# Performance work log

Measured on AMD Instinct MI355X. Metric: run time of the kernel, lower is better.

The kernel has to match this reference:

```python
import jax, jax.numpy as jnp
import numpy as np

B, S, HID = 1, 2048, 2048
NH, NKV, HD = 32, 8, 64  # query heads, kv heads, head dim
NEG = -1e9


def rotate_half(x):
    d = x.shape[-1] // 2
    return jnp.concatenate([-x[..., d:], x[..., :d]], axis=-1)


def setup_inputs() -> dict:
    key = jax.random.key(0)
    ks = jax.random.split(key, 8)
    hidden_states = jax.random.normal(ks[0], (B, S, HID), dtype=jnp.float32)
    # RoPE angles: realistic cos/sin tables (B, S, HD)
    inv_freq = 1.0 / (10000.0 ** (np.arange(0, HD, 2, dtype=np.float32) / HD))
    pos = np.arange(S, dtype=np.float32)
    ang = pos[:, None] * inv_freq[None, :]            # (S, HD/2)
    ang = np.concatenate([ang, ang], axis=-1)          # (S, HD)
    cos = jnp.broadcast_to(jnp.cos(ang)[None], (B, S, HD)).astype(jnp.float32)
    sin = jnp.broadcast_to(jnp.sin(ang)[None], (B, S, HD)).astype(jnp.float32)
    # additive causal mask (B, 1, S, S)
    causal = jnp.where(jnp.tril(jnp.ones((S, S), dtype=bool)), 0.0, NEG).astype(jnp.float32)
    attention_mask = jnp.broadcast_to(causal[None, None], (B, 1, S, S))
    std = 0.02
    Wq = jax.random.normal(ks[1], (NH * HD, HID), dtype=jnp.float32) * std
    Wk = jax.random.normal(ks[2], (NKV * HD, HID), dtype=jnp.float32) * std
    Wv = jax.random.normal(ks[3], (NKV * HD, HID), dtype=jnp.float32) * std
    Wo = jax.random.normal(ks[4], (HID, NH * HD), dtype=jnp.float32) * std
    return {"hidden_states": hidden_states, "cos": cos, "sin": sin,
            "attention_mask": attention_mask, "Wq": Wq, "Wk": Wk, "Wv": Wv, "Wo": Wo}


def reference(hidden_states, cos, sin, attention_mask, Wq, Wk, Wv, Wo):
    scaling = HD ** -0.5
    n_rep = NH // NKV
    # projections -> (B, H, S, D)
    q = jnp.einsum('bsh,qh->bsq', hidden_states, Wq).reshape(B, S, NH, HD).transpose(0, 2, 1, 3)
    k = jnp.einsum('bsh,qh->bsq', hidden_states, Wk).reshape(B, S, NKV, HD).transpose(0, 2, 1, 3)
    v = jnp.einsum('bsh,qh->bsq', hidden_states, Wv).reshape(B, S, NKV, HD).transpose(0, 2, 1, 3)
    # RoPE (cos/sin broadcast over head dim via [:, None])
    c, s = cos[:, None], sin[:, None]
    q = q * c + rotate_half(q) * s
    k = k * c + rotate_half(k) * s
    # GQA repeat_kv
    k = jnp.repeat(k, n_rep, axis=1)
    v = jnp.repeat(v, n_rep, axis=1)
    # eager attention
    attn_weights = jnp.einsum('bhqd,bhkd->bhqk', q, k) * scaling
    attn_weights = attn_weights + attention_mask
    attn_weights = jax.nn.softmax(attn_weights.astype(jnp.float32), axis=-1).astype(q.dtype)
    attn_output = jnp.einsum('bhqk,bhkd->bhqd', attn_weights, v)
    attn_output = attn_output.transpose(0, 2, 1, 3).reshape(B, S, NH * HD)
    attn_output = jnp.einsum('bsq,hq->bsh', attn_output, Wo)
    return attn_output, attn_weights
```

## Files before the change

kernel.cpp:

```cpp
#include <hip/hip_runtime.h>

#define S_LEN 2048
#define NH 32
#define NKV 8
#define HD 64
#define QH_DIM (NH * HD)
#define QKV_DIM 3072
#define K_OFF 2048
#define V_OFF 2560
#define LOG2E 1.44269504089f

typedef __attribute__((ext_vector_type(8))) __bf16 bf16x8;
typedef __attribute__((ext_vector_type(4))) float fx4;
typedef __attribute__((ext_vector_type(8))) unsigned short ush8;

__device__ __forceinline__ unsigned short f2bf(float f) {
  return __builtin_bit_cast(unsigned short, (__bf16)f);
}
__device__ __forceinline__ float bf2f(unsigned short h) {
  unsigned int u = ((unsigned int)h) << 16;
  return __builtin_bit_cast(float, u);
}
__device__ __forceinline__ fx4 zero4() {
  fx4 z; z[0] = 0.f; z[1] = 0.f; z[2] = 0.f; z[3] = 0.f; return z;
}

#define MFMA16(a, b, c) __builtin_amdgcn_mfma_f32_16x16x32_bf16((a), (b), (c), 0, 0, 0)

__device__ __forceinline__ void gl16(const void* g, void* l) {
  __builtin_amdgcn_global_load_lds((const __attribute__((address_space(1))) void*)g,
                                   (__attribute__((address_space(3))) void*)l, 16, 0, 0);
}

__global__ __launch_bounds__(256) void cast5(const float* __restrict__ s0, unsigned short* d0, int n0,
                                             const float* __restrict__ s1, unsigned short* d1, int n1,
                                             const float* __restrict__ s2, unsigned short* d2, int n2,
                                             const float* __restrict__ s3, unsigned short* d3, int n3,
                                             const float* __restrict__ s4, unsigned short* d4, int n4) {
  int i = blockIdx.x * 256 + threadIdx.x;
  const float* s;
  unsigned short* d;
  if (i < n0) { s = s0; d = d0; }
  else if ((i -= n0) < n1) { s = s1; d = d1; }
  else if ((i -= n1) < n2) { s = s2; d = d2; }
  else if ((i -= n2) < n3) { s = s3; d = d3; }
  else if ((i -= n3) < n4) { s = s4; d = d4; }
  else return;
  float4 v = ((const float4*)s)[i];
  ushort4 o;
  o.x = f2bf(v.x); o.y = f2bf(v.y); o.z = f2bf(v.z); o.w = f2bf(v.w);
  ((ushort4*)d)[i] = o;
}

__global__ __launch_bounds__(512) void gemm_split(const unsigned short* __restrict__ A,
                                                  const unsigned short* __restrict__ B,
                                                  unsigned short* __restrict__ Part,
                                                  int M, int N, int K) {
  __shared__ unsigned short As[2][128 * 32];
  __shared__ unsigned short Bs[2][128 * 32];
  const int tid = threadIdx.x;
  const int bn = blockIdx.x * 128, bm = blockIdx.y * 128;
  const int kslice = blockIdx.z;
  const int KH = K >> 1;
  const size_t koff = (size_t)kslice * KH;
  const int lane = tid & 63, wid = tid >> 6;
  const int lo = lane & 15, g = lane >> 4;
  const int wr = wid >> 2, wc = wid & 3;

  fx4 acc[4][2];
#pragma unroll
  for (int i = 0; i < 4; i++)
#pragma unroll
    for (int j = 0; j < 2; j++) acc[i][j] = zero4();

  const int srow = tid >> 2;
  const int cg = (tid & 3) ^ ((srow >> 1) & 3);
  const unsigned short* apg = &A[(size_t)(bm + srow) * K + koff + cg * 8];
  const unsigned short* bpg = &B[(size_t)(bn + srow) * K + koff + cg * 8];

  const int arow = wr * 64 + lo;
  const int brow = wc * 32 + lo;
  const int sc = (g ^ ((lo >> 1) & 3)) * 8;

#define G_STAGE(s, k0)                  \
  do {                                  \
    gl16(apg + (k0), &As[s][tid * 8]);  \
    gl16(bpg + (k0), &Bs[s][tid * 8]);  \
  } while (0)

#define G_COMPUTE(s)                                                   \
  do {                                                                 \
    bf16x8 af[4], bb[2];                                               \
    _Pragma("unroll") for (int mi = 0; mi < 4; mi++)                   \
        af[mi] = *(const bf16x8*)&As[s][(arow + mi * 16) * 32 + sc];   \
    _Pragma("unroll") for (int nj = 0; nj < 2; nj++)                   \
        bb[nj] = *(const bf16x8*)&Bs[s][(brow + nj * 16) * 32 + sc];   \
    _Pragma("unroll") for (int mi = 0; mi < 4; mi++)                   \
        _Pragma("unroll") for (int nj = 0; nj < 2; nj++)               \
            acc[mi][nj] = MFMA16(af[mi], bb[nj], acc[mi][nj]);         \
  } while (0)

  const int NT = KH >> 5;
  G_STAGE(0, 0);
  __syncthreads();
  int cur = 0;
  for (int t = 0; t < NT - 1; ++t) {
    G_STAGE(cur ^ 1, (t + 1) * 32);
    G_COMPUTE(cur);
    __syncthreads();
    cur ^= 1;
  }
  G_COMPUTE(cur);
#undef G_STAGE
#undef G_COMPUTE

  unsigned short* const pb = &Part[(size_t)kslice * M * N];
#pragma unroll
  for (int mi = 0; mi < 4; mi++)
#pragma unroll
    for (int nj = 0; nj < 2; nj++)
#pragma unroll
      for (int r = 0; r < 4; r++) {
        int row = bm + wr * 64 + mi * 16 + g * 4 + r;
        int col = bn + wc * 32 + nj * 16 + lo;
        pb[(size_t)row * N + col] = f2bf(acc[mi][nj][r]);
      }
}

__global__ __launch_bounds__(256) void combine_qkv(const unsigned short* __restrict__ P0,
                                                   const unsigned short* __restrict__ P1,
                                                   unsigned short* __restrict__ qkv,
                                                   const float* __restrict__ cosp,
                                                   const float* __restrict__ sinp,
                                                   unsigned short* __restrict__ Vt) {
  __shared__ unsigned short t[64][72];
  const int b = blockIdx.x;
  if (b < 2560) {
    int idx = b * 256 + threadIdx.x;
    int j = idx & 7;
    int tt = idx >> 3;
    int head = tt % 40;
    int s = tt / 40;
    const float scale = (head < 32) ? 0.125f * LOG2E : 1.0f;
    const size_t base = (size_t)s * QKV_DIM + head * 64 + j * 4;
    ushort4 a0l = *(const ushort4*)&P0[base];
    ushort4 a1l = *(const ushort4*)&P1[base];
    ushort4 a0h = *(const ushort4*)&P0[base + 32];
    ushort4 a1h = *(const ushort4*)&P1[base + 32];
    float xl0 = bf2f(a0l.x) + bf2f(a1l.x), xl1 = bf2f(a0l.y) + bf2f(a1l.y);
    float xl2 = bf2f(a0l.z) + bf2f(a1l.z), xl3 = bf2f(a0l.w) + bf2f(a1l.w);
    float xh0 = bf2f(a0h.x) + bf2f(a1h.x), xh1 = bf2f(a0h.y) + bf2f(a1h.y);
    float xh2 = bf2f(a0h.z) + bf2f(a1h.z), xh3 = bf2f(a0h.w) + bf2f(a1h.w);
    fx4 cl = *(const fx4*)&cosp[s * 64 + j * 4];
    fx4 ch = *(const fx4*)&cosp[s * 64 + 32 + j * 4];
    fx4 sl = *(const fx4*)&sinp[s * 64 + j * 4];
    fx4 sh = *(const fx4*)&sinp[s * 64 + 32 + j * 4];
    ushort4 ol, oh;
    ol.x = f2bf((xl0 * cl[0] - xh0 * sl[0]) * scale);
    ol.y = f2bf((xl1 * cl[1] - xh1 * sl[1]) * scale);
    ol.z = f2bf((xl2 * cl[2] - xh2 * sl[2]) * scale);
    ol.w = f2bf((xl3 * cl[3] - xh3 * sl[3]) * scale);
    oh.x = f2bf((xh0 * ch[0] + xl0 * sh[0]) * scale);
    oh.y = f2bf((xh1 * ch[1] + xl1 * sh[1]) * scale);
    oh.z = f2bf((xh2 * ch[2] + xl2 * sh[2]) * scale);
    oh.w = f2bf((xh3 * ch[3] + xl3 * sh[3]) * scale);
    *(ushort4*)&qkv[base] = ol;
    *(ushort4*)&qkv[base + 32] = oh;
  } else {
    const int tid = threadIdx.x;
    const int bb = b - 2560;
    const int cb = (bb & 7) * 64;
    const int rb = (bb >> 3) * 64;
#pragma unroll
    for (int rr = 0; rr < 2; rr++) {
      int row = rr * 32 + (tid >> 3);
      int c8 = (tid & 7) * 8;
      const size_t src = (size_t)(rb + row) * QKV_DIM + V_OFF + cb + c8;
      ush8 a = *(const ush8*)&P0[src];
      ush8 c = *(const ush8*)&P1[src];
      ush8 o;
#pragma unroll
      for (int j = 0; j < 8; j++) o[j] = f2bf(bf2f(a[j]) + bf2f(c[j]));
      *(ush8*)&t[row][c8] = o;
    }
    __syncthreads();
#pragma unroll
    for (int rr = 0; rr < 2; rr++) {
      int col = rr * 32 + (tid >> 3);
      int r8 = (tid & 7) * 8;
      ush8 o;
#pragma unroll
      for (int j = 0; j < 8; j++) o[j] = t[r8 + j][col];
      *(ush8*)&Vt[(size_t)(cb + col) * S_LEN + rb + r8] = o;
    }
  }
}

__global__ __launch_bounds__(256) void combine_wo(const unsigned short* __restrict__ P0,
                                                  const unsigned short* __restrict__ P1,
                                                  float* __restrict__ out) {
  const int i = blockIdx.x * 256 + threadIdx.x;
  const size_t base = (size_t)i * 8;
  ush8 a = *(const ush8*)&P0[base];
  ush8 b = *(const ush8*)&P1[base];
  fx4 o0, o1;
#pragma unroll
  for (int j = 0; j < 4; j++) o0[j] = bf2f(a[j]) + bf2f(b[j]);
#pragma unroll
  for (int j = 0; j < 4; j++) o1[j] = bf2f(a[4 + j]) + bf2f(b[4 + j]);
  *(fx4*)&out[base] = o0;
  *(fx4*)&out[base + 4] = o1;
}

__global__ __launch_bounds__(256) void attn_kernel(const unsigned short* __restrict__ Q,
                                                   const unsigned short* __restrict__ Kb,
                                                   const unsigned short* __restrict__ Vt,
                                                   float* __restrict__ P,
                                                   unsigned short* __restrict__ AO) {
  __shared__ unsigned short pls[16][2048];
  __shared__ float lred[4][16];
  const int h = blockIdx.x;
  const int rt = 127 - blockIdx.y;
  const int hkv = h >> 2;
  const int wid = threadIdx.x >> 6, lane = threadIdx.x & 63;
  const int lo = lane & 15, g = lane >> 4;
  const int rowb = rt * 16;
  const int nkt = (rt + 4) >> 2;
  const int qg = rowb + lo;
  char* const plsb = (char*)pls;
  const int swz = (lo & 7) << 4;

  {
    const int zc0 = nkt * 64;
    const int nz4 = (S_LEN - zc0) >> 2;
    for (int idx = threadIdx.x; idx < 16 * nz4; idx += 256) {
      const int r = idx / nz4;
      const int c = idx - r * nz4;
      __builtin_nontemporal_store(zero4(),
          (fx4*)&P[((size_t)h * S_LEN + rowb + r) * S_LEN + zc0 + c * 4]);
    }
  }

  const bf16x8 qa0 = *(const bf16x8*)&Q[(size_t)qg * QKV_DIM + h * HD + g * 8];
  const bf16x8 qa1 = *(const bf16x8*)&Q[(size_t)qg * QKV_DIM + h * HD + 32 + g * 8];

  float l = 0.f;
  {
    bf16x8 kc0[4], kc1[4];
    if (wid < nkt) {
#pragma unroll
      for (int nj = 0; nj < 4; nj++) {
        const int kcol = wid * 64 + nj * 16 + lo;
        kc0[nj] = *(const bf16x8*)&Kb[(size_t)kcol * QKV_DIM + hkv * HD + g * 8];
        kc1[nj] = *(const bf16x8*)&Kb[(size_t)kcol * QKV_DIM + hkv * HD + 32 + g * 8];
      }
    }
    for (int kt = wid; kt < nkt; kt += 4) {
      bf16x8 kn0[4], kn1[4];
      if (kt + 4 < nkt) {
#pragma unroll
        for (int nj = 0; nj < 4; nj++) {
          const int kcol = (kt + 4) * 64 + nj * 16 + lo;
          kn0[nj] = *(const bf16x8*)&Kb[(size_t)kcol * QKV_DIM + hkv * HD + g * 8];
          kn1[nj] = *(const bf16x8*)&Kb[(size_t)kcol * QKV_DIM + hkv * HD + 32 + g * 8];
        }
      }
      fx4 acc[4];
      __builtin_amdgcn_s_setprio(1);
#pragma unroll
      for (int nj = 0; nj < 4; nj++) {
        acc[nj] = MFMA16(kc0[nj], qa0, zero4());
        acc[nj] = MFMA16(kc1[nj], qa1, acc[nj]);
      }
      __builtin_amdgcn_s_setprio(0);
      const bool diag = (kt == nkt - 1);
#pragma unroll
      for (int nj = 0; nj < 4; nj++) {
        float e[4];
#pragma unroll
        for (int r = 0; r < 4; r++) {
          float v = exp2f(acc[nj][r]);
          if (diag && (kt * 64 + nj * 16 + g * 4 + r > qg)) v = 0.f;
          l += v;
          e[r] = v;
        }
        unsigned int w0 = (unsigned int)f2bf(e[0]) | ((unsigned int)f2bf(e[1]) << 16);
        unsigned int w1 = (unsigned int)f2bf(e[2]) | ((unsigned int)f2bf(e[3]) << 16);
        uint2 w; w.x = w0; w.y = w1;
        *(uint2*)(plsb + lo * 4096 + ((kt * 128 + nj * 32 + g * 8) ^ swz)) = w;
      }
#pragma unroll
      for (int j = 0; j < 4; j++) { kc0[j] = kn0[j]; kc1[j] = kn1[j]; }
    }
  }
  l += __shfl_xor(l, 16);
  l += __shfl_xor(l, 32);
  if (lane < 16) lred[wid][lo] = l;

  const unsigned short* const vrow = &Vt[(size_t)(hkv * HD + wid * 16 + lo) * S_LEN];
  bf16x8 vc0 = *(const bf16x8*)&vrow[g * 8];
  bf16x8 vc1 = *(const bf16x8*)&vrow[32 + g * 8];

  __syncthreads();

  float pinv[4];
#pragma unroll
  for (int it = 0; it < 4; it++) {
    const int rho = it * 4 + g;
    pinv[it] = 1.f / (lred[0][rho] + lred[1][rho] + lred[2][rho] + lred[3][rho]);
  }
  float* const pbase = &P[((size_t)h * S_LEN + rowb) * S_LEN];

  fx4 oacc = zero4();
  for (int kt = 0; kt < nkt; ++kt) {
    bf16x8 vn0, vn1;
    if (kt + 1 < nkt) {
      vn0 = *(const bf16x8*)&vrow[(kt + 1) * 64 + g * 8];
      vn1 = *(const bf16x8*)&vrow[(kt + 1) * 64 + 32 + g * 8];
    }
    bf16x8 pa0 = *(const bf16x8*)(plsb + lo * 4096 + ((kt * 128 + g * 16) ^ swz));
    bf16x8 pa1 = *(const bf16x8*)(plsb + lo * 4096 + ((kt * 128 + 64 + g * 16) ^ swz));
    __builtin_amdgcn_s_setprio(1);
    oacc = MFMA16(pa0, vc0, oacc);
    oacc = MFMA16(pa1, vc1, oacc);
    __builtin_amdgcn_s_setprio(0);
    if ((kt & 3) == wid) {
#pragma unroll
      for (int it = 0; it < 4; it++) {
        const int rho = it * 4 + g;
        ushort4 b4 = *(const ushort4*)(plsb + rho * 4096 +
                                       ((kt * 128 + lo * 8) ^ ((rho & 7) << 4)));
        fx4 pv;
        pv[0] = bf2f(b4.x) * pinv[it]; pv[1] = bf2f(b4.y) * pinv[it];
        pv[2] = bf2f(b4.z) * pinv[it]; pv[3] = bf2f(b4.w) * pinv[it];
        __builtin_nontemporal_store(pv,
            (fx4*)&pbase[(size_t)rho * S_LEN + kt * 64 + lo * 4]);
      }
    }
    vc0 = vn0; vc1 = vn1;
  }

#pragma unroll
  for (int r = 0; r < 4; r++) {
    const int q = g * 4 + r;
    const float linv = 1.f / (lred[0][q] + lred[1][q] + lred[2][q] + lred[3][q]);
    AO[(size_t)(rowb + q) * QH_DIM + h * HD + wid * 16 + lo] = f2bf(oacc[r] * linv);
  }
}

extern "C" void kernel_launch(void* const* d_in, const int* in_sizes, int n_in,
                              void* d_out, int out_size, void* d_ws, size_t ws_size,
                              hipStream_t stream) {
  const float* hs = (const float*)d_in[0];
  const float* cosp = (const float*)d_in[1];
  const float* sinp = (const float*)d_in[2];
  const float* Wq = (const float*)d_in[4];
  const float* Wk = (const float*)d_in[5];
  const float* Wv = (const float*)d_in[6];
  const float* Wo = (const float*)d_in[7];

  char* w = (char*)d_ws;
  unsigned short* wo_bf   = (unsigned short*)(w);
  unsigned short* ao_bf   = (unsigned short*)(w + (((size_t)9) << 20));
  unsigned short* hs_bf   = (unsigned short*)(w + (((size_t)18) << 20));
  unsigned short* wqkv_bf = (unsigned short*)(w + (((size_t)27) << 20));
  unsigned short* qkv_bf  = (unsigned short*)(w + (((size_t)40) << 20));
  unsigned short* vt_bf   = (unsigned short*)(w + (((size_t)53) << 20));
  unsigned short* wop     = hs_bf;

  float* out0 = (float*)d_out;
  float* P = out0 + (size_t)S_LEN * QH_DIM;
  const size_t P_BYTES = (size_t)NH * S_LEN * S_LEN * 4;
  const size_t QKVP_BYTES = (size_t)2 * S_LEN * QKV_DIM * 2;
  unsigned short* qkvp = (unsigned short*)((char*)P + P_BYTES - QKVP_BYTES);

  cast5<<<14336, 256, 0, stream>>>(hs, hs_bf, 1048576,
                                   Wq, wqkv_bf, 1048576,
                                   Wk, wqkv_bf + (size_t)K_OFF * 2048, 262144,
                                   Wv, wqkv_bf + (size_t)V_OFF * 2048, 262144,
                                   Wo, wo_bf, 1048576);

  gemm_split<<<dim3(QKV_DIM / 128, 16, 2), 512, 0, stream>>>(hs_bf, wqkv_bf, qkvp,
                                                             2048, QKV_DIM, 2048);

  combine_qkv<<<2816, 256, 0, stream>>>(qkvp, qkvp + (size_t)S_LEN * QKV_DIM,
                                        qkv_bf, cosp, sinp, vt_bf);

  attn_kernel<<<dim3(NH, 128), 256, 0, stream>>>(qkv_bf, qkv_bf + K_OFF, vt_bf, P, ao_bf);

  gemm_split<<<dim3(16, 16, 2), 512, 0, stream>>>(ao_bf, wo_bf, wop, 2048, 2048, 2048);

  combine_wo<<<2048, 256, 0, stream>>>(wop, wop + (size_t)S_LEN * QH_DIM, out0);
}
```

Before: 260.4 us.

## Use eight waves per attention block with split-K PV and LDS reduction

Attention blocks grow from 4 to 8 waves. The QK tiles are strided across 8 waves, and the PV accumulation is split into two parity halves over key tiles. The halves are combined through a shared-memory buffer before writing the attention output. The goal is more latency hiding per block on the exp/store-heavy path; the cost is an extra sync, extra LDS, and fewer registers per thread. The GEMM launch bounds also gain a min-blocks hint, which may constrain registers.

```diff
diff --git a/kernel.cpp b/kernel.cpp
--- a/kernel.cpp
+++ b/kernel.cpp
@@ -52,10 +52,10 @@
   ((ushort4*)d)[i] = o;
 }
 
-__global__ __launch_bounds__(512) void gemm_split(const unsigned short* __restrict__ A,
-                                                  const unsigned short* __restrict__ B,
-                                                  unsigned short* __restrict__ Part,
-                                                  int M, int N, int K) {
+__global__ __launch_bounds__(512, 6) void gemm_split(const unsigned short* __restrict__ A,
+                                                     const unsigned short* __restrict__ B,
+                                                     unsigned short* __restrict__ Part,
+                                                     int M, int N, int K) {
   __shared__ unsigned short As[2][128 * 32];
   __shared__ unsigned short Bs[2][128 * 32];
   const int tid = threadIdx.x;
@@ -212,13 +212,14 @@
   *(fx4*)&out[base + 4] = o1;
 }
 
-__global__ __launch_bounds__(256) void attn_kernel(const unsigned short* __restrict__ Q,
-                                                   const unsigned short* __restrict__ Kb,
-                                                   const unsigned short* __restrict__ Vt,
-                                                   float* __restrict__ P,
-                                                   unsigned short* __restrict__ AO) {
+__global__ __launch_bounds__(512, 4) void attn_kernel(const unsigned short* __restrict__ Q,
+                                                      const unsigned short* __restrict__ Kb,
+                                                      const unsigned short* __restrict__ Vt,
+                                                      float* __restrict__ P,
+                                                      unsigned short* __restrict__ AO) {
   __shared__ unsigned short pls[16][2048];
-  __shared__ float lred[4][16];
+  __shared__ float lred[8][16];
+  __shared__ fx4 obuf[4][64];
   const int h = blockIdx.x;
   const int rt = 127 - blockIdx.y;
   const int hkv = h >> 2;
@@ -233,7 +234,7 @@
   {
     const int zc0 = nkt * 64;
     const int nz4 = (S_LEN - zc0) >> 2;
-    for (int idx = threadIdx.x; idx < 16 * nz4; idx += 256) {
+    for (int idx = threadIdx.x; idx < 16 * nz4; idx += 512) {
       const int r = idx / nz4;
       const int c = idx - r * nz4;
       __builtin_nontemporal_store(zero4(),
@@ -255,12 +256,12 @@
         kc1[nj] = *(const bf16x8*)&Kb[(size_t)kcol * QKV_DIM + hkv * HD + 32 + g * 8];
       }
     }
-    for (int kt = wid; kt < nkt; kt += 4) {
+    for (int kt = wid; kt < nkt; kt += 8) {
       bf16x8 kn0[4], kn1[4];
-      if (kt + 4 < nkt) {
+      if (kt + 8 < nkt) {
 #pragma unroll
         for (int nj = 0; nj < 4; nj++) {
-          const int kcol = (kt + 4) * 64 + nj * 16 + lo;
+          const int kcol = (kt + 8) * 64 + nj * 16 + lo;
           kn0[nj] = *(const bf16x8*)&Kb[(size_t)kcol * QKV_DIM + hkv * HD + g * 8];
           kn1[nj] = *(const bf16x8*)&Kb[(size_t)kcol * QKV_DIM + hkv * HD + 32 + g * 8];
         }
@@ -297,9 +298,11 @@
   l += __shfl_xor(l, 32);
   if (lane < 16) lred[wid][lo] = l;
 
-  const unsigned short* const vrow = &Vt[(size_t)(hkv * HD + wid * 16 + lo) * S_LEN];
-  bf16x8 vc0 = *(const bf16x8*)&vrow[g * 8];
-  bf16x8 vc1 = *(const bf16x8*)&vrow[32 + g * 8];
+  const int d0 = (wid & 3) * 16;
+  const int par = wid >> 2;
+  const unsigned short* const vrow = &Vt[(size_t)(hkv * HD + d0 + lo) * S_LEN];
+  bf16x8 vc0 = *(const bf16x8*)&vrow[par * 64 + g * 8];
+  bf16x8 vc1 = *(const bf16x8*)&vrow[par * 64 + 32 + g * 8];
 
   __syncthreads();
 
@@ -307,16 +310,17 @@
 #pragma unroll
   for (int it = 0; it < 4; it++) {
     const int rho = it * 4 + g;
-    pinv[it] = 1.f / (lred[0][rho] + lred[1][rho] + lred[2][rho] + lred[3][rho]);
+    pinv[it] = 1.f / (lred[0][rho] + lred[1][rho] + lred[2][rho] + lred[3][rho] +
+                      lred[4][rho] + lred[5][rho] + lred[6][rho] + lred[7][rho]);
   }
   float* const pbase = &P[((size_t)h * S_LEN + rowb) * S_LEN];
 
   fx4 oacc = zero4();
-  for (int kt = 0; kt < nkt; ++kt) {
+  for (int kt = par; kt < nkt; kt += 2) {
     bf16x8 vn0, vn1;
-    if (kt + 1 < nkt) {
-      vn0 = *(const bf16x8*)&vrow[(kt + 1) * 64 + g * 8];
-      vn1 = *(const bf16x8*)&vrow[(kt + 1) * 64 + 32 + g * 8];
+    if (kt + 2 < nkt) {
+      vn0 = *(const bf16x8*)&vrow[(kt + 2) * 64 + g * 8];
+      vn1 = *(const bf16x8*)&vrow[(kt + 2) * 64 + 32 + g * 8];
     }
     bf16x8 pa0 = *(const bf16x8*)(plsb + lo * 4096 + ((kt * 128 + g * 16) ^ swz));
     bf16x8 pa1 = *(const bf16x8*)(plsb + lo * 4096 + ((kt * 128 + 64 + g * 16) ^ swz));
@@ -324,7 +328,7 @@
     oacc = MFMA16(pa0, vc0, oacc);
     oacc = MFMA16(pa1, vc1, oacc);
     __builtin_amdgcn_s_setprio(0);
-    if ((kt & 3) == wid) {
+    if (((kt >> 1) & 3) == (wid & 3)) {
 #pragma unroll
       for (int it = 0; it < 4; it++) {
         const int rho = it * 4 + g;
@@ -340,11 +344,17 @@
     vc0 = vn0; vc1 = vn1;
   }
 
-#pragma unroll
-  for (int r = 0; r < 4; r++) {
-    const int q = g * 4 + r;
-    const float linv = 1.f / (lred[0][q] + lred[1][q] + lred[2][q] + lred[3][q]);
-    AO[(size_t)(rowb + q) * QH_DIM + h * HD + wid * 16 + lo] = f2bf(oacc[r] * linv);
+  if (par == 1) obuf[wid & 3][lane] = oacc;
+  __syncthreads();
+  if (par == 0) {
+    fx4 o2 = obuf[wid][lane];
+#pragma unroll
+    for (int r = 0; r < 4; r++) {
+      const int q = g * 4 + r;
+      const float linv = 1.f / (lred[0][q] + lred[1][q] + lred[2][q] + lred[3][q] +
+                                lred[4][q] + lred[5][q] + lred[6][q] + lred[7][q]);
+      AO[(size_t)(rowb + q) * QH_DIM + h * HD + d0 + lo] = f2bf((oacc[r] + o2[r]) * linv);
+    }
   }
 }
 
@@ -386,7 +396,7 @@
   combine_qkv<<<2816, 256, 0, stream>>>(qkvp, qkvp + (size_t)S_LEN * QKV_DIM,
                                         qkv_bf, cosp, sinp, vt_bf);
 
-  attn_kernel<<<dim3(NH, 128), 256, 0, stream>>>(qkv_bf, qkv_bf + K_OFF, vt_bf, P, ao_bf);
+  attn_kernel<<<dim3(NH, 128), 512, 0, stream>>>(qkv_bf, qkv_bf + K_OFF, vt_bf, P, ao_bf);
 
   gemm_split<<<dim3(16, 16, 2), 512, 0, stream>>>(ao_bf, wo_bf, wop, 2048, 2048, 2048);
 
```

Result: faster. 253.5 us (-2.7%).
